# Kernel optimization log

Hardware: AMD Instinct MI355X
Metric: run time of the kernel (lower is better)

The kernel has to match this reference:

```python
import jax, jax.numpy as jnp
import numpy as np

B, S, D = 2, 2048, 512   # batch, seq_len, input_dim
H, E = 8, 512            # num_heads, per-head output_dim (full D per head, per source)
NEG = -1e9


def setup_inputs() -> dict:
    key = jax.random.key(0)
    ks = jax.random.split(key, 12)
    sc = 1.0 / np.sqrt(D)
    inp = {
        "query": jax.random.normal(ks[0], (B, S, D), jnp.float32),
        "key":   jax.random.normal(ks[1], (B, S, D), jnp.float32),
        "value": jax.random.normal(ks[2], (B, S, D), jnp.float32),
        "mask":  jax.random.randint(ks[3], (B, S, S), 0, 2).astype(bool),
        # stacked per-head Linear weights: [H, D, E] (x @ W layout)
        "Wq": jax.random.normal(ks[4], (H, D, E), jnp.float32) * sc,
        "bq": jax.random.normal(ks[5], (H, E), jnp.float32) * 0.02,
        "Wk": jax.random.normal(ks[6], (H, D, E), jnp.float32) * sc,
        "bk": jax.random.normal(ks[7], (H, E), jnp.float32) * 0.02,
        "Wv": jax.random.normal(ks[8], (H, D, E), jnp.float32) * sc,
        "bv": jax.random.normal(ks[9], (H, E), jnp.float32) * 0.02,
        # output projection: Linear(H*E, E)
        "Wo": jax.random.normal(ks[10], (H * E, E), jnp.float32) * (1.0 / np.sqrt(H * E)),
        "bo": jax.random.normal(ks[11], (E,), jnp.float32) * 0.02,
    }
    return inp


def reference(query, key, value, mask, Wq, bq, Wk, bk, Wv, bv, Wo, bo):
    # Batched per-head projections (replaces the Python per-head loop)
    q = jnp.einsum("bsd,hde->bhse", query, Wq) + bq[None, :, None, :]
    k = jnp.einsum("bsd,hde->bhse", key,   Wk) + bk[None, :, None, :]
    v = jnp.einsum("bsd,hde->bhse", value, Wv) + bv[None, :, None, :]
    # NOTE: source has NO 1/sqrt(d) scaling — kept faithful.
    scores = jnp.einsum("bhse,bhte->bhst", q, k)           # [B,H,S,S]
    scores = jnp.where(mask[:, None, :, :], scores, NEG)    # masked_fill(mask==0, -1e9)
    attn = jax.nn.softmax(scores, axis=-1)
    out = jnp.einsum("bhst,bhte->bhse", attn, v)            # [B,H,S,E]
    # concat heads along last dim in head order -> [B,S,H*E]
    cat = out.transpose(0, 2, 1, 3).reshape(out.shape[0], out.shape[2], -1)
    return cat @ Wo + bo
```

## Files before the change

kernel.cpp:

```cpp
#include <hip/hip_runtime.h>

#define B_  2
#define S_  2048
#define D_  512
#define H_  8
#define E_  512
#define HE_ 4096

typedef _Float16 half8_t  __attribute__((ext_vector_type(8)));
typedef _Float16 half4_t  __attribute__((ext_vector_type(4)));
typedef float    floatx4  __attribute__((ext_vector_type(4)));
typedef __attribute__((address_space(1))) const unsigned int* gas_ptr;
typedef __attribute__((address_space(3))) unsigned int*       las_ptr;

__global__ __launch_bounds__(256) void cast3_f16_kernel(
    const float* __restrict__ s0, const float* __restrict__ s1, const float* __restrict__ s2,
    _Float16* __restrict__ d0, _Float16* __restrict__ d1, _Float16* __restrict__ d2, int n4) {
    int i = blockIdx.x * 256 + threadIdx.x;
    if (i >= n4) return;
    const float* s = (blockIdx.y == 0) ? s0 : (blockIdx.y == 1) ? s1 : s2;
    _Float16*    d = (blockIdx.y == 0) ? d0 : (blockIdx.y == 1) ? d1 : d2;
    float4 v = ((const float4*)s)[i];
    half4_t h = { (_Float16)v.x, (_Float16)v.y, (_Float16)v.z, (_Float16)v.w };
    ((half4_t*)d)[i] = h;
}

__global__ __launch_bounds__(256) void transpose3_cast_kernel(
    const float* __restrict__ p0, const float* __restrict__ p1, const float* __restrict__ p2,
    _Float16* __restrict__ q0, _Float16* __restrict__ q1, _Float16* __restrict__ q2,
    int R, int C) {
    __shared__ float t[32][33];
    int which = blockIdx.z >> 3, hh = blockIdx.z & 7;
    const float* src = ((which == 0) ? p0 : (which == 1) ? p1 : p2) + (long long)hh * R * C;
    _Float16*    dst = ((which == 0) ? q0 : (which == 1) ? q1 : q2) + (long long)hh * R * C;
    int c0 = blockIdx.x * 32, r0 = blockIdx.y * 32;
    int tx = threadIdx.x, ty = threadIdx.y;
#pragma unroll
    for (int i = 0; i < 32; i += 8)
        t[ty + i][tx] = src[(long long)(r0 + ty + i) * C + (c0 + tx)];
    __syncthreads();
#pragma unroll
    for (int i = 0; i < 32; i += 8)
        dst[(long long)(c0 + ty + i) * R + (r0 + tx)] = (_Float16)t[tx][ty + i];
}

__global__ __launch_bounds__(256) void transpose_cast_kernel(const float* __restrict__ src,
                                                             _Float16* __restrict__ dst,
                                                             int R, int C) {
    __shared__ float t[32][33];
    int c0 = blockIdx.x * 32, r0 = blockIdx.y * 32;
    int tx = threadIdx.x, ty = threadIdx.y;
#pragma unroll
    for (int i = 0; i < 32; i += 8)
        t[ty + i][tx] = src[(long long)(r0 + ty + i) * C + (c0 + tx)];
    __syncthreads();
#pragma unroll
    for (int i = 0; i < 32; i += 8)
        dst[(long long)(c0 + ty + i) * R + (r0 + tx)] = (_Float16)t[tx][ty + i];
}


__global__ __launch_bounds__(256) void gemm_qkv_kernel(
    const _Float16* __restrict__ Xq, const _Float16* __restrict__ Xk, const _Float16* __restrict__ Xv,
    const _Float16* __restrict__ WqT, const _Float16* __restrict__ WkT, const _Float16* __restrict__ WvT,
    const float* __restrict__ bq, const float* __restrict__ bk, const float* __restrict__ bv,
    _Float16* __restrict__ Qb, _Float16* __restrict__ Kb, _Float16* __restrict__ VT)
{
    int z = blockIdx.z;
    int which = z >> 4, zz = z & 15;
    int bb = zz >> 3, hh = zz & 7;
    const _Float16* A  = ((which == 0) ? Xq : (which == 1) ? Xk : Xv) + (long long)bb * S_ * D_;
    const _Float16* Bt = ((which == 0) ? WqT : (which == 1) ? WkT : WvT) + (long long)hh * E_ * D_;
    const float* bias  = ((which == 0) ? bq : (which == 1) ? bk : bv) + hh * E_;

    int m0 = blockIdx.y * 128;
    int n0 = blockIdx.x * 128;

    __shared__ __align__(16) _Float16 As[2][128][32];
    __shared__ __align__(16) _Float16 Bs[2][128][32];

    int tid  = threadIdx.x;
    int wave = tid >> 6, lane = tid & 63;
    int quad = lane >> 4, l16 = lane & 15;
    int wy = (wave >> 1) * 64, wx = (wave & 1) * 64;
    int pw = wave & 1, rw = (wave >> 1) * 64;
    int sr = lane >> 2;
    int scg = ((lane & 3) ^ ((lane >> 3) & 3)) * 8;
    _Float16* lA0 = &As[pw][rw][0];
    _Float16* lB0 = &Bs[pw][rw][0];
    int cra = (quad ^ ((l16 >> 1) & 3)) * 8;

    floatx4 acc[4][4] = {};

    for (int k0 = 0; k0 < D_; k0 += 64) {
        if (k0) __syncthreads();
        const _Float16* gA = A + (long long)(m0 + rw + sr) * D_ + k0 + pw * 32 + scg;
        const _Float16* gB = Bt + (long long)(n0 + rw + sr) * D_ + k0 + pw * 32 + scg;
#pragma unroll
        for (int j = 0; j < 4; j++) {
            __builtin_amdgcn_global_load_lds((gas_ptr)(gA + (long long)(j * 16) * D_),
                                             (las_ptr)(lA0 + j * 512), 16, 0, 0);
            __builtin_amdgcn_global_load_lds((gas_ptr)(gB + (long long)(j * 16) * D_),
                                             (las_ptr)(lB0 + j * 512), 16, 0, 0);
        }
        __syncthreads();
#pragma unroll
        for (int kc = 0; kc < 2; kc++) {
            half8_t af[4], bf[4];
#pragma unroll
            for (int i = 0; i < 4; i++) {
                af[i] = *(const half8_t*)&As[kc][wy + i * 16 + l16][cra];
                bf[i] = *(const half8_t*)&Bs[kc][wx + i * 16 + l16][cra];
            }
#pragma unroll
            for (int mi = 0; mi < 4; mi++)
#pragma unroll
                for (int ni = 0; ni < 4; ni++)
                    acc[mi][ni] = __builtin_amdgcn_mfma_f32_16x16x32_f16(af[mi], bf[ni], acc[mi][ni], 0, 0, 0);
        }
    }

    if (which < 2) {
        _Float16* C = ((which == 0) ? Qb : Kb) + ((long long)(bb * H_ + hh)) * S_ * E_;
#pragma unroll
        for (int mi = 0; mi < 4; mi++)
#pragma unroll
            for (int ni = 0; ni < 4; ni++)
#pragma unroll
                for (int r = 0; r < 4; r++) {
                    int row = m0 + wy + mi * 16 + quad * 4 + r;
                    int col = n0 + wx + ni * 16 + l16;
                    C[(long long)row * E_ + col] = (_Float16)(acc[mi][ni][r] + bias[col]);
                }
    } else {
        _Float16* C = VT + ((long long)(bb * H_ + hh)) * E_ * S_;
#pragma unroll
        for (int mi = 0; mi < 4; mi++)
#pragma unroll
            for (int ni = 0; ni < 4; ni++) {
                int row = m0 + wy + mi * 16 + quad * 4;
                int col = n0 + wx + ni * 16 + l16;
                float bcol = bias[col];
                half4_t h4 = { (_Float16)(acc[mi][ni][0] + bcol), (_Float16)(acc[mi][ni][1] + bcol),
                               (_Float16)(acc[mi][ni][2] + bcol), (_Float16)(acc[mi][ni][3] + bcol) };
                *(half4_t*)(C + (long long)col * S_ + row) = h4;
            }
    }
}

__global__ __launch_bounds__(256) void gemm_bt_kernel(
    const _Float16* __restrict__ A, const _Float16* __restrict__ Bt,
    _Float16* __restrict__ C,
    int K, int lda, int ldb,
    long long a_z, long long b_z, long long c_b, long long c_h, int c_rs, int hdiv)
{
    int z = blockIdx.z;
    int bb = z / hdiv, hh = z % hdiv;
    A  += (long long)z * a_z;
    Bt += (long long)z * b_z;
    _Float16* Cz = C + bb * c_b + hh * c_h;

    int m0 = blockIdx.y * 128;
    int n0 = blockIdx.x * 128;

    __shared__ __align__(16) _Float16 As[2][128][32];
    __shared__ __align__(16) _Float16 Bs[2][128][32];

    int tid  = threadIdx.x;
    int wave = tid >> 6, lane = tid & 63;
    int quad = lane >> 4, l16 = lane & 15;
    int wy = (wave >> 1) * 64, wx = (wave & 1) * 64;
    int pw = wave & 1, rw = (wave >> 1) * 64;
    int sr = lane >> 2;
    int scg = ((lane & 3) ^ ((lane >> 3) & 3)) * 8;
    _Float16* lA0 = &As[pw][rw][0];
    _Float16* lB0 = &Bs[pw][rw][0];
    int cra = (quad ^ ((l16 >> 1) & 3)) * 8;

    floatx4 acc[4][4] = {};

    for (int k0 = 0; k0 < K; k0 += 64) {
        if (k0) __syncthreads();
        const _Float16* gA = A + (long long)(m0 + rw + sr) * lda + k0 + pw * 32 + scg;
        const _Float16* gB = Bt + (long long)(n0 + rw + sr) * ldb + k0 + pw * 32 + scg;
#pragma unroll
        for (int j = 0; j < 4; j++) {
            __builtin_amdgcn_global_load_lds((gas_ptr)(gA + (long long)(j * 16) * lda),
                                             (las_ptr)(lA0 + j * 512), 16, 0, 0);
            __builtin_amdgcn_global_load_lds((gas_ptr)(gB + (long long)(j * 16) * ldb),
                                             (las_ptr)(lB0 + j * 512), 16, 0, 0);
        }
        __syncthreads();
#pragma unroll
        for (int kc = 0; kc < 2; kc++) {
            half8_t af[4], bf[4];
#pragma unroll
            for (int i = 0; i < 4; i++) {
                af[i] = *(const half8_t*)&As[kc][wy + i * 16 + l16][cra];
                bf[i] = *(const half8_t*)&Bs[kc][wx + i * 16 + l16][cra];
            }
#pragma unroll
            for (int mi = 0; mi < 4; mi++)
#pragma unroll
                for (int ni = 0; ni < 4; ni++)
                    acc[mi][ni] = __builtin_amdgcn_mfma_f32_16x16x32_f16(af[mi], bf[ni], acc[mi][ni], 0, 0, 0);
        }
    }

#pragma unroll
    for (int mi = 0; mi < 4; mi++)
#pragma unroll
        for (int ni = 0; ni < 4; ni++)
#pragma unroll
            for (int r = 0; r < 4; r++) {
                int row = m0 + wy + mi * 16 + quad * 4 + r;
                int col = n0 + wx + ni * 16 + l16;
                Cz[(long long)row * c_rs + col] = (_Float16)acc[mi][ni][r];
            }
}

__global__ __launch_bounds__(512) void softmax_mask8_kernel(_Float16* __restrict__ sc,
                                                            const int* __restrict__ mask)
{
    int b = blockIdx.z, s = blockIdx.x;
    int wave = threadIdx.x >> 6, lane = threadIdx.x & 63;
    _Float16* row = sc + ((long long)(b * H_ + wave) * S_ + s) * S_;
    const int* mrow = mask + ((long long)b * S_ + s) * S_;

    half8_t h[4];
    float v[32];
    float mx = -3.0e38f;
#pragma unroll
    for (int j = 0; j < 4; j++) {
        int c = j * 512 + lane * 8;
        h[j] = *(const half8_t*)(row + c);
        int4 mA = *(const int4*)(mrow + c);
        int4 mB = *(const int4*)(mrow + c + 4);
        int mm[8] = { mA.x, mA.y, mA.z, mA.w, mB.x, mB.y, mB.z, mB.w };
#pragma unroll
        for (int e = 0; e < 8; e++) {
            float val = mm[e] ? (float)h[j][e] : -1.0e9f;
            v[j * 8 + e] = val;
            mx = fmaxf(mx, val);
        }
    }
#pragma unroll
    for (int o = 32; o > 0; o >>= 1) mx = fmaxf(mx, __shfl_xor(mx, o));

    float sum = 0.0f;
#pragma unroll
    for (int i = 0; i < 32; i++) { v[i] = __expf(v[i] - mx); sum += v[i]; }
#pragma unroll
    for (int o = 32; o > 0; o >>= 1) sum += __shfl_xor(sum, o);

    float inv = 1.0f / sum;
#pragma unroll
    for (int j = 0; j < 4; j++) {
#pragma unroll
        for (int e = 0; e < 8; e++) h[j][e] = (_Float16)(v[j * 8 + e] * inv);
        *(half8_t*)(row + j * 512 + lane * 8) = h[j];
    }
}

__global__ __launch_bounds__(256) void gemm_bt_n64_splitk_kernel(
    const _Float16* __restrict__ A, const _Float16* __restrict__ Bt,
    const float* __restrict__ bias, float* __restrict__ C,
    int K, int lda, int ldb, int ldc, int ksplit)
{
    int m0 = blockIdx.y * 128;
    int n0 = blockIdx.x * 64;
    int kchunk = K / ksplit;
    int kbeg = blockIdx.z * kchunk;
    int kend = kbeg + kchunk;

    __shared__ __align__(16) _Float16 As[128][32];
    __shared__ __align__(16) _Float16 Bs[64][32];

    int tid  = threadIdx.x;
    int wave = tid >> 6, lane = tid & 63;
    int quad = lane >> 4, l16 = lane & 15;
    int wy = (wave >> 1) * 64, wx = (wave & 1) * 32;

    int srow = (wave << 4) + (lane >> 2);
    int scg = ((lane & 3) ^ ((lane >> 3) & 3)) * 8;
    _Float16* lA0 = &As[0][0] + (wave << 9);
    _Float16* lB0 = &Bs[0][0] + (wave << 9);
    int cra = (quad ^ ((l16 >> 1) & 3)) * 8;

    floatx4 acc[4][2] = {};

    for (int k0 = kbeg; k0 < kend; k0 += 32) {
        if (k0 != kbeg) __syncthreads();
        const _Float16* gA = A + (long long)(m0 + srow) * lda + k0 + scg;
        const _Float16* gB = Bt + (long long)(n0 + srow) * ldb + k0 + scg;
#pragma unroll
        for (int j = 0; j < 2; j++)
            __builtin_amdgcn_global_load_lds((gas_ptr)(gA + (long long)(j << 6) * lda),
                                             (las_ptr)(lA0 + (j << 11)), 16, 0, 0);
        __builtin_amdgcn_global_load_lds((gas_ptr)gB, (las_ptr)lB0, 16, 0, 0);
        __syncthreads();

        half8_t af[4], bf[2];
#pragma unroll
        for (int i = 0; i < 4; i++)
            af[i] = *(const half8_t*)&As[wy + i * 16 + l16][cra];
#pragma unroll
        for (int i = 0; i < 2; i++)
            bf[i] = *(const half8_t*)&Bs[wx + i * 16 + l16][cra];
#pragma unroll
        for (int mi = 0; mi < 4; mi++)
#pragma unroll
            for (int ni = 0; ni < 2; ni++)
                acc[mi][ni] = __builtin_amdgcn_mfma_f32_16x16x32_f16(af[mi], bf[ni], acc[mi][ni], 0, 0, 0);
    }

    int addb = (blockIdx.z == 0) && bias;
#pragma unroll
    for (int mi = 0; mi < 4; mi++)
#pragma unroll
        for (int ni = 0; ni < 2; ni++)
#pragma unroll
            for (int r = 0; r < 4; r++) {
                int row = m0 + wy + mi * 16 + quad * 4 + r;
                int col = n0 + wx + ni * 16 + l16;
                float v = acc[mi][ni][r];
                if (addb) v += bias[col];
                atomicAdd(&C[(long long)row * ldc + col], v);
            }
}

extern "C" void kernel_launch(void* const* d_in, const int* in_sizes, int n_in,
                              void* d_out, int out_size, void* d_ws, size_t ws_size,
                              hipStream_t stream)
{
    const float* qin = (const float*)d_in[0];
    const float* kin = (const float*)d_in[1];
    const float* vin = (const float*)d_in[2];
    const int*   mask = (const int*)d_in[3];
    const float* Wq = (const float*)d_in[4];
    const float* bq = (const float*)d_in[5];
    const float* Wk = (const float*)d_in[6];
    const float* bk = (const float*)d_in[7];
    const float* Wv = (const float*)d_in[8];
    const float* bv = (const float*)d_in[9];
    const float* Wo = (const float*)d_in[10];
    const float* bo = (const float*)d_in[11];
    float* out = (float*)d_out;

    char* ws = (char*)d_ws;
    size_t off = 0;
    _Float16* WoT = (_Float16*)(ws + off); off += (size_t)E_ * HE_ * 2;
    _Float16* Qb  = (_Float16*)(ws + off); off += (size_t)B_ * H_ * S_ * E_ * 2;
    _Float16* Kb  = (_Float16*)(ws + off); off += (size_t)B_ * H_ * S_ * E_ * 2;
    _Float16* VT  = (_Float16*)(ws + off); off += (size_t)B_ * H_ * E_ * S_ * 2;
    size_t region = off;
    _Float16* Xq  = (_Float16*)(ws + region);
    _Float16* Xk  = Xq  + (size_t)B_ * S_ * D_;
    _Float16* Xv  = Xk  + (size_t)B_ * S_ * D_;
    _Float16* WqT = Xv  + (size_t)B_ * S_ * D_;
    _Float16* WkT = WqT + (size_t)H_ * E_ * D_;
    _Float16* WvT = WkT + (size_t)H_ * E_ * D_;
    _Float16* SC  = (_Float16*)(ws + region);
    _Float16* cat = Qb;

    long long SE = (long long)S_ * E_;
    long long SS = (long long)S_ * S_;
    long long ES = (long long)E_ * S_;

    (void)hipMemsetAsync(d_out, 0, (size_t)out_size * sizeof(float), stream);

    int n4 = B_ * S_ * D_ / 4;
    cast3_f16_kernel<<<dim3(n4 / 256, 3), 256, 0, stream>>>(qin, kin, vin, Xq, Xk, Xv, n4);

    dim3 tb(32, 8);
    transpose3_cast_kernel<<<dim3(E_ / 32, D_ / 32, 24), tb, 0, stream>>>(
        Wq, Wk, Wv, WqT, WkT, WvT, D_, E_);
    transpose_cast_kernel<<<dim3(E_ / 32, HE_ / 32, 1), tb, 0, stream>>>(Wo, WoT, HE_, E_);

    gemm_qkv_kernel<<<dim3(E_ / 128, S_ / 128, 48), 256, 0, stream>>>(
        Xq, Xk, Xv, WqT, WkT, WvT, bq, bk, bv, Qb, Kb, VT);

    gemm_bt_kernel<<<dim3(S_ / 128, S_ / 128, B_ * H_), 256, 0, stream>>>(
        Qb, Kb, SC, E_, E_, E_, SE, SE, 0, SS, S_, 32 );

    softmax_mask8_kernel<<<dim3(S_, 1, B_), 512, 0, stream>>>(SC, mask);

    gemm_bt_kernel<<<dim3(E_ / 128, S_ / 128, B_ * H_), 256, 0, stream>>>(
        SC, VT, cat, S_, S_, S_, SS, ES, (long long)S_ * HE_, E_, HE_, H_);

    gemm_bt_n64_splitk_kernel<<<dim3(E_ / 64, (B_ * S_) / 128, 4), 256, 0, stream>>>(
        cat, WoT, bo, out, HE_, HE_, HE_, E_, 4);
}
```

Baseline: 489.4 us.

## Use 256x256 tiled GEMM with 4-stage LDS pipeline and XCD-aware block mapping

Replaces the 128x128 double-buffered batched GEMM used for QK^T and attn·V with a 512-thread, 256x256-tile kernel that streams K-slices of 32 through a 4-deep LDS ring, using explicit vmcnt waits and raw barriers. It also adds a block-index remap that groups consecutive batch/head slices onto the same XCD, and applies that remap to the QKV projection too. The goal is more data reuse per tile, fewer barriers, load latency hidden behind MFMA, and better L2 locality per XCD. In exchange it uses far more LDS and registers (32 accumulators per lane), and the attn·V grid shrinks to 2x8x16 blocks, which may underfill the GPU.

```diff
diff --git a/kernel.cpp b/kernel.cpp
--- a/kernel.cpp
+++ b/kernel.cpp
@@ -60,21 +60,38 @@
 }
 
 
+__device__ __forceinline__ void xcd_decode(int& z, int& by, int& bx) {
+    int gx = gridDim.x, gy = gridDim.y, gz = gridDim.z;
+    int bpz = gx * gy;
+    int fid = blockIdx.x + gx * (blockIdx.y + gy * blockIdx.z);
+    if ((gz & 7) == 0) {
+        int xcd = fid & 7, sl = fid >> 3;
+        int zg = gz >> 3;
+        z = xcd * zg + sl / bpz;
+        int inner = sl % bpz;
+        by = inner / gx;
+        bx = inner % gx;
+    } else {
+        z = blockIdx.z; by = blockIdx.y; bx = blockIdx.x;
+    }
+}
+
 __global__ __launch_bounds__(256) void gemm_qkv_kernel(
     const _Float16* __restrict__ Xq, const _Float16* __restrict__ Xk, const _Float16* __restrict__ Xv,
     const _Float16* __restrict__ WqT, const _Float16* __restrict__ WkT, const _Float16* __restrict__ WvT,
     const float* __restrict__ bq, const float* __restrict__ bk, const float* __restrict__ bv,
     _Float16* __restrict__ Qb, _Float16* __restrict__ Kb, _Float16* __restrict__ VT)
 {
-    int z = blockIdx.z;
+    int z, byy, bxx;
+    xcd_decode(z, byy, bxx);
     int which = z >> 4, zz = z & 15;
     int bb = zz >> 3, hh = zz & 7;
     const _Float16* A  = ((which == 0) ? Xq : (which == 1) ? Xk : Xv) + (long long)bb * S_ * D_;
     const _Float16* Bt = ((which == 0) ? WqT : (which == 1) ? WkT : WvT) + (long long)hh * E_ * D_;
     const float* bias  = ((which == 0) ? bq : (which == 1) ? bk : bv) + hh * E_;
 
-    int m0 = blockIdx.y * 128;
-    int n0 = blockIdx.x * 128;
+    int m0 = byy * 128;
+    int n0 = bxx * 128;
 
     __shared__ __align__(16) _Float16 As[2][128][32];
     __shared__ __align__(16) _Float16 Bs[2][128][32];
@@ -148,73 +165,94 @@
     }
 }
 
-__global__ __launch_bounds__(256) void gemm_bt_kernel(
+__global__ __launch_bounds__(512, 2) void gemm_bt256_kernel(
     const _Float16* __restrict__ A, const _Float16* __restrict__ Bt,
     _Float16* __restrict__ C,
     int K, int lda, int ldb,
     long long a_z, long long b_z, long long c_b, long long c_h, int c_rs, int hdiv)
 {
-    int z = blockIdx.z;
+    int z, byy, bxx;
+    xcd_decode(z, byy, bxx);
     int bb = z / hdiv, hh = z % hdiv;
     A  += (long long)z * a_z;
     Bt += (long long)z * b_z;
     _Float16* Cz = C + bb * c_b + hh * c_h;
 
-    int m0 = blockIdx.y * 128;
-    int n0 = blockIdx.x * 128;
-
-    __shared__ __align__(16) _Float16 As[2][128][32];
-    __shared__ __align__(16) _Float16 Bs[2][128][32];
+    int m0 = byy * 256;
+    int n0 = bxx * 256;
+
+    __shared__ __align__(16) _Float16 As[4][256][32];
+    __shared__ __align__(16) _Float16 Bs[4][256][32];
 
     int tid  = threadIdx.x;
     int wave = tid >> 6, lane = tid & 63;
     int quad = lane >> 4, l16 = lane & 15;
-    int wy = (wave >> 1) * 64, wx = (wave & 1) * 64;
-    int pw = wave & 1, rw = (wave >> 1) * 64;
+    int wm128 = (wave >> 2) * 128;
+    int wn64  = (wave & 3) * 64;
+    int wave16 = wave * 16;
     int sr = lane >> 2;
     int scg = ((lane & 3) ^ ((lane >> 3) & 3)) * 8;
-    _Float16* lA0 = &As[pw][rw][0];
-    _Float16* lB0 = &Bs[pw][rw][0];
     int cra = (quad ^ ((l16 >> 1) & 3)) * 8;
 
-    floatx4 acc[4][4] = {};
-
-    for (int k0 = 0; k0 < K; k0 += 64) {
-        if (k0) __syncthreads();
-        const _Float16* gA = A + (long long)(m0 + rw + sr) * lda + k0 + pw * 32 + scg;
-        const _Float16* gB = Bt + (long long)(n0 + rw + sr) * ldb + k0 + pw * 32 + scg;
-#pragma unroll
-        for (int j = 0; j < 4; j++) {
-            __builtin_amdgcn_global_load_lds((gas_ptr)(gA + (long long)(j * 16) * lda),
-                                             (las_ptr)(lA0 + j * 512), 16, 0, 0);
-            __builtin_amdgcn_global_load_lds((gas_ptr)(gB + (long long)(j * 16) * ldb),
-                                             (las_ptr)(lB0 + j * 512), 16, 0, 0);
+    auto STAGE = [&](int t) {
+        int buf = t & 3;
+        int kk = t << 5;
+        const _Float16* gA = A + (long long)(m0 + wave16 + sr) * lda + kk + scg;
+        const _Float16* gB = Bt + (long long)(n0 + wave16 + sr) * ldb + kk + scg;
+        _Float16* lA = &As[buf][wave16][0];
+        _Float16* lB = &Bs[buf][wave16][0];
+#pragma unroll
+        for (int j = 0; j < 2; j++) {
+            __builtin_amdgcn_global_load_lds((gas_ptr)(gA + (long long)(j * 128) * lda),
+                                             (las_ptr)(lA + j * 128 * 32), 16, 0, 0);
+            __builtin_amdgcn_global_load_lds((gas_ptr)(gB + (long long)(j * 128) * ldb),
+                                             (las_ptr)(lB + j * 128 * 32), 16, 0, 0);
         }
-        __syncthreads();
-#pragma unroll
-        for (int kc = 0; kc < 2; kc++) {
-            half8_t af[4], bf[4];
-#pragma unroll
-            for (int i = 0; i < 4; i++) {
-                af[i] = *(const half8_t*)&As[kc][wy + i * 16 + l16][cra];
-                bf[i] = *(const half8_t*)&Bs[kc][wx + i * 16 + l16][cra];
-            }
-#pragma unroll
-            for (int mi = 0; mi < 4; mi++)
-#pragma unroll
-                for (int ni = 0; ni < 4; ni++)
-                    acc[mi][ni] = __builtin_amdgcn_mfma_f32_16x16x32_f16(af[mi], bf[ni], acc[mi][ni], 0, 0, 0);
+    };
+
+    int nt = K >> 5;
+
+    STAGE(0);
+    if (nt > 1) STAGE(1);
+    if (nt > 2) STAGE(2);
+    if (nt > 2)      asm volatile("s_waitcnt vmcnt(8)" ::: "memory");
+    else if (nt > 1) asm volatile("s_waitcnt vmcnt(4)" ::: "memory");
+    else             asm volatile("s_waitcnt vmcnt(0)" ::: "memory");
+    __builtin_amdgcn_s_barrier();
+
+    floatx4 acc[8][4] = {};
+
+    for (int t = 0; t < nt; ++t) {
+        if (t + 3 < nt) STAGE(t + 3);
+        int buf = t & 3;
+        half8_t af[8], bf[4];
+#pragma unroll
+        for (int i = 0; i < 8; i++)
+            af[i] = *(const half8_t*)&As[buf][wm128 + i * 16 + l16][cra];
+#pragma unroll
+        for (int i = 0; i < 4; i++)
+            bf[i] = *(const half8_t*)&Bs[buf][wn64 + i * 16 + l16][cra];
+#pragma unroll
+        for (int mi = 0; mi < 8; mi++)
+#pragma unroll
+            for (int ni = 0; ni < 4; ni++)
+                acc[mi][ni] = __builtin_amdgcn_mfma_f32_16x16x32_f16(af[mi], bf[ni], acc[mi][ni], 0, 0, 0);
+        if (t + 1 < nt) {
+            if (t + 3 < nt)      asm volatile("s_waitcnt vmcnt(8) lgkmcnt(0)" ::: "memory");
+            else if (t + 2 < nt) asm volatile("s_waitcnt vmcnt(4) lgkmcnt(0)" ::: "memory");
+            else                 asm volatile("s_waitcnt vmcnt(0) lgkmcnt(0)" ::: "memory");
+            __builtin_amdgcn_s_barrier();
         }
     }
 
 #pragma unroll
-    for (int mi = 0; mi < 4; mi++)
+    for (int mi = 0; mi < 8; mi++)
 #pragma unroll
         for (int ni = 0; ni < 4; ni++)
 #pragma unroll
             for (int r = 0; r < 4; r++) {
-                int row = m0 + wy + mi * 16 + quad * 4 + r;
-                int col = n0 + wx + ni * 16 + l16;
+                int row = m0 + wm128 + mi * 16 + quad * 4 + r;
+                int col = n0 + wn64 + ni * 16 + l16;
                 Cz[(long long)row * c_rs + col] = (_Float16)acc[mi][ni][r];
             }
 }
@@ -380,12 +418,12 @@
     gemm_qkv_kernel<<<dim3(E_ / 128, S_ / 128, 48), 256, 0, stream>>>(
         Xq, Xk, Xv, WqT, WkT, WvT, bq, bk, bv, Qb, Kb, VT);
 
-    gemm_bt_kernel<<<dim3(S_ / 128, S_ / 128, B_ * H_), 256, 0, stream>>>(
+    gemm_bt256_kernel<<<dim3(S_ / 256, S_ / 256, B_ * H_), 512, 0, stream>>>(
         Qb, Kb, SC, E_, E_, E_, SE, SE, 0, SS, S_, 32 );
 
     softmax_mask8_kernel<<<dim3(S_, 1, B_), 512, 0, stream>>>(SC, mask);
 
-    gemm_bt_kernel<<<dim3(E_ / 128, S_ / 128, B_ * H_), 256, 0, stream>>>(
+    gemm_bt256_kernel<<<dim3(E_ / 256, S_ / 256, B_ * H_), 512, 0, stream>>>(
         SC, VT, cat, S_, S_, S_, SS, ES, (long long)S_ * HE_, E_, HE_, H_);
 
     gemm_bt_n64_splitk_kernel<<<dim3(E_ / 64, (B_ * S_) / 128, 4), 256, 0, stream>>>(
```

Result: slower. 533.3 us (+9.0%).
